# Kernel tuning notes

Measured on AMD Instinct MI355X. Metric: run time of the kernel, lower is better.

Reference implementation:

```python
import jax, jax.numpy as jnp
import numpy as np

B, N, DIM = 4, 4096, 1024
HEADS, DFF, WIN = 16, 4096, 128
EPS = 1e-5


def _layernorm(x, w, b):
    mu = jnp.mean(x, axis=-1, keepdims=True)
    var = jnp.mean(jnp.square(x - mu), axis=-1, keepdims=True)
    return (x - mu) * jax.lax.rsqrt(var + EPS) * w + b


def _local_attention(q, k, v, window):
    # q,k,v: (B, h, N, d); non-causal, look_backward=1, look_forward=1
    Bq, h, n, d = q.shape
    nb = n // window
    scale = d ** -0.5
    q = q.reshape(Bq * h, nb, window, d) * scale
    k = k.reshape(Bq * h, nb, window, d)
    v = v.reshape(Bq * h, nb, window, d)

    def look_around(t):  # (BH, nb, w, d) -> (BH, nb, 3w, d)
        tp = jnp.pad(t, ((0, 0), (1, 1), (0, 0), (0, 0)))
        return jnp.concatenate([tp[:, :-2], tp[:, 1:-1], tp[:, 2:]], axis=2)

    kk = look_around(k)
    vv = look_around(v)

    # validity mask for out-of-range look-around buckets
    idx = jnp.arange(n).reshape(nb, window)
    idx_p = jnp.pad(idx, ((1, 1), (0, 0)), constant_values=-1)
    kidx = jnp.concatenate([idx_p[:-2], idx_p[1:-1], idx_p[2:]], axis=1)  # (nb, 3w)
    valid = (kidx >= 0)[None, :, None, :]  # (1, nb, 1, 3w)

    sim = jnp.einsum('bnid,bnjd->bnij', q, kk)  # (BH, nb, w, 3w)
    neg = jnp.finfo(sim.dtype).min
    sim = jnp.where(valid, sim, neg)
    attn = jax.nn.softmax(sim, axis=-1)
    out = jnp.einsum('bnij,bnjd->bnid', attn, vv)
    return out.reshape(Bq, h, n, d)


def setup_inputs() -> dict:
    key = jax.random.key(0)
    ks = jax.random.split(key, 8)
    w = lambda k, shape: jax.random.normal(k, shape, jnp.float32) * 0.02
    return {
        'x': jax.random.normal(ks[0], (B, N, DIM), jnp.float32),
        'ln1_w': jnp.ones((DIM,), jnp.float32), 'ln1_b': jnp.zeros((DIM,), jnp.float32),
        'qkv_w': w(ks[1], (3 * DIM, DIM)), 'qkv_b': jnp.zeros((3 * DIM,), jnp.float32),
        'proj_w': w(ks[2], (DIM, DIM)), 'proj_b': jnp.zeros((DIM,), jnp.float32),
        'ln2_w': jnp.ones((DIM,), jnp.float32), 'ln2_b': jnp.zeros((DIM,), jnp.float32),
        'fc1_w': w(ks[3], (DFF, DIM)), 'fc1_b': jnp.zeros((DFF,), jnp.float32),
        'fc2_w': w(ks[4], (DIM, DFF)), 'fc2_b': jnp.zeros((DIM,), jnp.float32),
    }


def reference(x, ln1_w, ln1_b, qkv_w, qkv_b, proj_w, proj_b, ln2_w, ln2_b, fc1_w, fc1_b, fc2_w, fc2_b):
    Bx, n, C = x.shape
    h = HEADS
    hd = C // h
    x_norm = _layernorm(x, ln1_w, ln1_b)
    qkv = x_norm @ qkv_w.T + qkv_b  # (B, N, 3C)
    qkv = qkv.reshape(Bx, n, 3, h, hd).transpose(2, 0, 3, 1, 4)  # (3, B, h, N, hd)
    q, k, v = qkv[0], qkv[1], qkv[2]
    attn_out = _local_attention(q, k, v, WIN)  # (B, h, N, hd)
    attn_out = attn_out.transpose(0, 2, 1, 3).reshape(Bx, n, C)
    x = x + (attn_out @ proj_w.T + proj_b)
    y = _layernorm(x, ln2_w, ln2_b)
    y = jax.nn.gelu(y @ fc1_w.T + fc1_b, approximate=False)
    x = x + (y @ fc2_w.T + fc2_b)
    return x
```

## Files before the change

### kernel.cpp

```cpp
#include <hip/hip_runtime.h>
#include <math.h>

typedef unsigned short u16;
typedef __attribute__((ext_vector_type(4))) float f32x4;
typedef __attribute__((ext_vector_type(8))) __bf16 bf16x8;
typedef __attribute__((ext_vector_type(8))) u16 u16x8;
typedef __attribute__((ext_vector_type(4))) u16 u16x4;

__device__ __forceinline__ float bf2f(u16 v) {
    unsigned int u = ((unsigned int)v) << 16;
    return __builtin_bit_cast(float, u);
}
__device__ __forceinline__ u16 f2bf(float f) {
    unsigned int x = __builtin_bit_cast(unsigned int, f);
    x += 0x7fffu + ((x >> 16) & 1u);
    return (u16)(x >> 16);
}

__device__ __forceinline__ void load_lds16(const u16* g, u16* l) {
    __builtin_amdgcn_global_load_lds((const __attribute__((address_space(1))) void*)g,
                                     (__attribute__((address_space(3))) void*)l, 16, 0, 0);
}

#define WAIT_VM(N) asm volatile("s_waitcnt vmcnt(" #N ")" ::: "memory")
#define MFMA16(d, x, y) d = __builtin_amdgcn_mfma_f32_16x16x32_bf16(x, y, d, 0, 0, 0)

__device__ __forceinline__ void phase_barrier() {
    __builtin_amdgcn_sched_barrier(0);
    asm volatile("" ::: "memory");
    __builtin_amdgcn_s_barrier();
    asm volatile("" ::: "memory");
    __builtin_amdgcn_sched_barrier(0);
}

__global__ __launch_bounds__(256) void cvt_kernel(const float* __restrict__ in,
                                                  u16* __restrict__ out, int n)
{
    const int i = (blockIdx.x * 256 + threadIdx.x) * 4;
    if (i >= n) return;
    const float4 f = *(const float4*)(in + i);
    u16x4 o;
    o[0] = f2bf(f.x); o[1] = f2bf(f.y); o[2] = f2bf(f.z); o[3] = f2bf(f.w);
    *(u16x4*)(out + i) = o;
}

template<int EPI, int RES, bool OF32>
__global__ __launch_bounds__(512, 2) void gemm256(
    const u16* __restrict__ A, const u16* __restrict__ W,
    const float* __restrict__ bias,
    const float* __restrict__ resf, const u16* __restrict__ resb,
    void* __restrict__ O0v, u16* __restrict__ O1, u16* __restrict__ O2,
    int M, int N, int K, int mbase)
{
    __shared__ u16 S[65536];
    const int tid  = threadIdx.x;
    const int w    = tid >> 6;
    const int l    = tid & 63;
    const int colq = l & 15;
    const int quad = l >> 4;
    const int w3   = w & 3;
    const int wm   = (w >> 2) * 128;
    const int wn   = w3 * 64;

    const int nX  = (int)gridDim.x;
    const int nwg = nX * (int)gridDim.y;
    const int did = (int)blockIdx.y * nX + (int)blockIdx.x;
    const int q8  = nwg >> 3;
    const int wg  = (nwg & 7) ? did : ((did & 7) * q8 + (did >> 3));
    const int bm  = wg / nX;
    const int bn  = wg - bm * nX;
    const int m0  = bm * 256, n0 = bn * 256;

    const int rw   = l >> 3;
    const int sseg = ((l & 7) ^ rw) * 8;
    const u16* gA[2][2];
    const u16* gB[2][2];
#pragma unroll
    for (int h = 0; h < 2; ++h)
#pragma unroll
        for (int j = 0; j < 2; ++j) {
            const int rr = (w * 2 + j) * 8 + rw;
            gA[h][j] = A + (size_t)(m0 + h * 128 + rr) * K + sseg;
            const int nl = (rr >> 5) * 64 + (h * 2 + ((rr >> 4) & 1)) * 16 + (rr & 15);
            gB[h][j] = W + (size_t)(n0 + nl) * K + sseg;
        }
    const int lw = w * 1024;

    const int c0   = (quad * 8) ^ ((colq & 7) << 3);
    const int c1   = c0 ^ 32;
    const int aoff = (wm + colq) * 64;
    const int boff = 16384 + (w3 * 32 + colq) * 64;

    f32x4 acc[8][4] = {};
    bf16x8 a0[8], a1[8], b0, b1;

#pragma unroll
    for (int h = 0; h < 2; ++h)
#pragma unroll
        for (int j = 0; j < 2; ++j)
            load_lds16(gA[h][j], S + h * 8192 + lw + j * 512);
#pragma unroll
    for (int h = 0; h < 2; ++h)
#pragma unroll
        for (int j = 0; j < 2; ++j)
            load_lds16(gB[h][j], S + 16384 + h * 8192 + lw + j * 512);
    WAIT_VM(2);
    phase_barrier();

    const int NT = K >> 6;
    for (int t = 0; t < NT; ++t) {
        u16* Sc = S + ((t & 1) << 15);
        u16* Sn = S + (((t + 1) & 1) << 15);
        const int  kk = (t + 1) << 6;
        const bool pf = (t + 1) < NT;

#pragma unroll
        for (int mf = 0; mf < 8; ++mf)
            a0[mf] = *(const bf16x8*)(Sc + aoff + mf * 1024 + c0);
        b0 = *(const bf16x8*)(Sc + boff + c0);
        b1 = *(const bf16x8*)(Sc + boff + 1024 + c0);
        if (pf) {
#pragma unroll
            for (int h = 0; h < 2; ++h)
#pragma unroll
                for (int j = 0; j < 2; ++j)
                    load_lds16(gA[h][j] + kk, Sn + h * 8192 + lw + j * 512);
        }
        __builtin_amdgcn_s_setprio(1);
#pragma unroll
        for (int mf = 0; mf < 8; ++mf) { MFMA16(acc[mf][0], a0[mf], b0); MFMA16(acc[mf][1], a0[mf], b1); }
        __builtin_amdgcn_s_setprio(0);
        phase_barrier();

#pragma unroll
        for (int mf = 0; mf < 8; ++mf)
            a1[mf] = *(const bf16x8*)(Sc + aoff + mf * 1024 + c1);
        b0 = *(const bf16x8*)(Sc + boff + c1);
        b1 = *(const bf16x8*)(Sc + boff + 1024 + c1);
        if (pf) {
#pragma unroll
            for (int j = 0; j < 2; ++j)
                load_lds16(gB[0][j] + kk, Sn + 16384 + lw + j * 512);
        }
        __builtin_amdgcn_s_setprio(1);
#pragma unroll
        for (int mf = 0; mf < 8; ++mf) { MFMA16(acc[mf][0], a1[mf], b0); MFMA16(acc[mf][1], a1[mf], b1); }
        __builtin_amdgcn_s_setprio(0);
        if (pf) { WAIT_VM(6); } else { WAIT_VM(0); }
        phase_barrier();

        b0 = *(const bf16x8*)(Sc + boff + 8192 + c0);
        b1 = *(const bf16x8*)(Sc + boff + 8192 + 1024 + c0);
        if (pf) {
#pragma unroll
            for (int j = 0; j < 2; ++j)
                load_lds16(gB[1][j] + kk, Sn + 16384 + 8192 + lw + j * 512);
        }
        __builtin_amdgcn_s_setprio(1);
#pragma unroll
        for (int mf = 0; mf < 8; ++mf) { MFMA16(acc[mf][2], a0[mf], b0); MFMA16(acc[mf][3], a0[mf], b1); }
        __builtin_amdgcn_s_setprio(0);
        phase_barrier();

        b0 = *(const bf16x8*)(Sc + boff + 8192 + c1);
        b1 = *(const bf16x8*)(Sc + boff + 8192 + 1024 + c1);
        __builtin_amdgcn_s_setprio(1);
#pragma unroll
        for (int mf = 0; mf < 8; ++mf) { MFMA16(acc[mf][2], a1[mf], b0); MFMA16(acc[mf][3], a1[mf], b1); }
        __builtin_amdgcn_s_setprio(0);
        if (pf) { WAIT_VM(2); }
        phase_barrier();
    }

#pragma unroll
    for (int nf = 0; nf < 4; ++nf) {
        const int c = n0 + wn + nf * 16 + colq;
        const float bz = bias[c];
#pragma unroll
        for (int mf = 0; mf < 8; ++mf) {
#pragma unroll
            for (int i = 0; i < 4; ++i) {
                const int r = m0 + wm + mf * 16 + quad * 4 + i;
                float v = acc[mf][nf][i] + bz;
                if constexpr (EPI == 0) {
                    const int which = c >> 10;
                    const int head  = (c >> 6) & 15;
                    const int d     = c & 63;
                    const int rg    = mbase + r;
                    const int bb    = rg >> 12;
                    const int tt    = rg & 4095;
                    const int bh    = bb * 16 + head;
                    const u16 val = f2bf(v);
                    if (which == 0)      ((u16*)O0v)[((size_t)bh * 4096 + tt) * 64 + d] = val;
                    else if (which == 1) O1[((size_t)bh * 4096 + tt) * 64 + d] = val;
                    else                 O2[((size_t)bh * 64 + d) * 4096 + tt] = val;
                } else {
                    const size_t idx = (size_t)r * N + c;
                    if constexpr (RES == 1) v += resf[idx];
                    if constexpr (RES == 2) v += bf2f(resb[idx]);
                    if constexpr (EPI == 2) v = 0.5f * v * (1.0f + erff(v * 0.70710678118654752f));
                    if constexpr (OF32) ((float*)O0v)[idx] = v;
                    else                ((u16*)O0v)[idx] = f2bf(v);
                }
            }
        }
    }
}

template<bool F32IN>
__global__ __launch_bounds__(256) void ln_kernel(
    const void* __restrict__ xin, const float* __restrict__ w,
    const float* __restrict__ b, u16* __restrict__ out)
{
    const int wave = threadIdx.x >> 6, lane = threadIdx.x & 63;
    const size_t row = (size_t)blockIdx.x * 4 + wave;
    float v[16];
    if constexpr (F32IN) {
        const float* xr = (const float*)xin + row * 1024 + lane * 16;
#pragma unroll
        for (int j = 0; j < 4; ++j) {
            const float4 f = *(const float4*)(xr + j * 4);
            v[j * 4 + 0] = f.x; v[j * 4 + 1] = f.y; v[j * 4 + 2] = f.z; v[j * 4 + 3] = f.w;
        }
    } else {
        const u16* xr = (const u16*)xin + row * 1024 + lane * 16;
        u16x8 xa = *(const u16x8*)xr;
        u16x8 xb = *(const u16x8*)(xr + 8);
#pragma unroll
        for (int i = 0; i < 8; ++i) { v[i] = bf2f(xa[i]); v[8 + i] = bf2f(xb[i]); }
    }
    float s = 0.f, s2 = 0.f;
#pragma unroll
    for (int i = 0; i < 16; ++i) { s += v[i]; s2 += v[i] * v[i]; }
#pragma unroll
    for (int m = 32; m >= 1; m >>= 1) { s += __shfl_xor(s, m, 64); s2 += __shfl_xor(s2, m, 64); }
    const float mu  = s * (1.0f / 1024.0f);
    const float var = s2 * (1.0f / 1024.0f) - mu * mu;
    const float rs  = rsqrtf(var + 1e-5f);
    const float* wp = w + lane * 16;
    const float* bp = b + lane * 16;
    u16x8 oa, ob;
#pragma unroll
    for (int i = 0; i < 8; ++i) {
        oa[i] = f2bf((v[i]     - mu) * rs * wp[i]     + bp[i]);
        ob[i] = f2bf((v[8 + i] - mu) * rs * wp[8 + i] + bp[8 + i]);
    }
    u16* orow = out + row * 1024 + lane * 16;
    *(u16x8*)orow       = oa;
    *(u16x8*)(orow + 8) = ob;
}

__global__ __launch_bounds__(256, 4) void attn_kernel(
    const u16* __restrict__ Q, const u16* __restrict__ Kb,
    const u16* __restrict__ Vt, u16* __restrict__ out)
{
    __shared__ u16 Ps[4][16 * 200];
    const int tid  = threadIdx.x;
    const int wave = tid >> 6;
    const int lane = tid & 63;
    const int colq = lane & 15;
    const int quad = lane >> 4;

    const int f   = blockIdx.x;
    const int xcd = f & 7;
    const int s8  = f >> 3;
    const int bh  = s8 >> 3;
    const int tb  = (s8 & 7) + 8 * xcd;
    const int qrow0 = tb * 64 + wave * 16;
    const int nb    = tb >> 1;
    const int key0  = nb * 128 - 128;
    const int nt_lo = (nb == 0) ? 8 : 0;
    const int nt_hi = (nb == 31) ? 16 : 24;

    const u16* qp = Q + ((size_t)bh * 4096 + qrow0 + colq) * 64 + quad * 8;
    bf16x8 aq0 = *(const bf16x8*)qp;
    bf16x8 aq1 = *(const bf16x8*)(qp + 32);

    float m_i[4], l_i[4];
    f32x4 o[4] = {};
#pragma unroll
    for (int i = 0; i < 4; ++i) { m_i[i] = -3.0e38f; l_i[i] = 0.f; }

    u16* Psw = &Ps[wave][0];

#pragma unroll
    for (int c = 0; c < 2; ++c) {
        const int lo = (c == 0) ? nt_lo : 12;
        const int hi = (c == 0) ? ((nt_hi < 12) ? nt_hi : 12) : nt_hi;

        f32x4 sc[12];
#pragma unroll
        for (int j = 0; j < 12; ++j) sc[j] = (f32x4){0.f, 0.f, 0.f, 0.f};
#pragma unroll
        for (int j = 0; j < 12; ++j) {
            const int nt = c * 12 + j;
            if (nt >= lo && nt < hi) {
                const u16* kp = Kb + ((size_t)bh * 4096 + key0 + nt * 16 + colq) * 64 + quad * 8;
                bf16x8 b0 = *(const bf16x8*)kp;
                bf16x8 b1 = *(const bf16x8*)(kp + 32);
                f32x4 z = {0.f, 0.f, 0.f, 0.f};
                z = __builtin_amdgcn_mfma_f32_16x16x32_bf16(aq0, b0, z, 0, 0, 0);
                z = __builtin_amdgcn_mfma_f32_16x16x32_bf16(aq1, b1, z, 0, 0, 0);
                sc[j] = z;
            }
        }
        float mc[4];
#pragma unroll
        for (int i = 0; i < 4; ++i) mc[i] = -3.0e38f;
#pragma unroll
        for (int j = 0; j < 12; ++j) {
            const int nt = c * 12 + j;
            if (nt >= lo && nt < hi)
#pragma unroll
                for (int i = 0; i < 4; ++i) mc[i] = fmaxf(mc[i], sc[j][i]);
        }
#pragma unroll
        for (int i = 0; i < 4; ++i)
#pragma unroll
            for (int m = 8; m >= 1; m >>= 1) mc[i] = fmaxf(mc[i], __shfl_xor(mc[i], m, 64));
        float a_i[4], psum[4];
#pragma unroll
        for (int i = 0; i < 4; ++i) {
            const float mn = fmaxf(m_i[i], mc[i]);
            a_i[i] = __expf((m_i[i] - mn) * 0.125f);
            m_i[i] = mn;
            psum[i] = 0.f;
        }
#pragma unroll
        for (int j = 0; j < 12; ++j) {
            const int nt = c * 12 + j;
            if (nt >= lo && nt < hi) {
#pragma unroll
                for (int i = 0; i < 4; ++i) {
                    const float p = __expf((sc[j][i] - m_i[i]) * 0.125f);
                    psum[i] += p;
                    Psw[(quad * 4 + i) * 200 + j * 16 + colq] = f2bf(p);
                }
            }
        }
#pragma unroll
        for (int i = 0; i < 4; ++i)
#pragma unroll
            for (int m = 8; m >= 1; m >>= 1) psum[i] += __shfl_xor(psum[i], m, 64);
#pragma unroll
        for (int i = 0; i < 4; ++i) l_i[i] = l_i[i] * a_i[i] + psum[i];
#pragma unroll
        for (int dt = 0; dt < 4; ++dt)
#pragma unroll
            for (int i = 0; i < 4; ++i) o[dt][i] *= a_i[i];
        const int klo = (lo - c * 12) >> 1;
        const int khi = (hi - c * 12) >> 1;
#pragma unroll
        for (int k6 = 0; k6 < 6; ++k6) {
            if (k6 >= klo && k6 < khi) {
                bf16x8 ap = *(const bf16x8*)(Psw + colq * 200 + k6 * 32 + quad * 8);
                const int kkk = key0 + (c * 6 + k6) * 32 + quad * 8;
#pragma unroll
                for (int dt = 0; dt < 4; ++dt) {
                    const u16* vp = Vt + ((size_t)bh * 64 + dt * 16 + colq) * 4096 + kkk;
                    bf16x8 bv = *(const bf16x8*)vp;
                    o[dt] = __builtin_amdgcn_mfma_f32_16x16x32_bf16(ap, bv, o[dt], 0, 0, 0);
                }
            }
        }
    }

    const int bb = bh >> 4, hh = bh & 15;
#pragma unroll
    for (int i = 0; i < 4; ++i) {
        const float inv = 1.0f / fmaxf(l_i[i], 1e-20f);
        const int t = qrow0 + quad * 4 + i;
        u16* op = out + ((size_t)(bb * 4096 + t)) * 1024 + hh * 64;
#pragma unroll
        for (int dt = 0; dt < 4; ++dt) op[dt * 16 + colq] = f2bf(o[dt][i] * inv);
    }
}

extern "C" void kernel_launch(void* const* d_in, const int* in_sizes, int n_in,
                              void* d_out, int out_size, void* d_ws, size_t ws_size,
                              hipStream_t stream)
{
    const float* x      = (const float*)d_in[0];
    const float* ln1_w  = (const float*)d_in[1];
    const float* ln1_b  = (const float*)d_in[2];
    const float* qkv_w  = (const float*)d_in[3];
    const float* qkv_b  = (const float*)d_in[4];
    const float* proj_w = (const float*)d_in[5];
    const float* proj_b = (const float*)d_in[6];
    const float* ln2_w  = (const float*)d_in[7];
    const float* ln2_b  = (const float*)d_in[8];
    const float* fc1_w  = (const float*)d_in[9];
    const float* fc1_b  = (const float*)d_in[10];
    const float* fc2_w  = (const float*)d_in[11];
    const float* fc2_b  = (const float*)d_in[12];
    float* outp = (float*)d_out;

    if (ws_size < 134217728u) return;
    char* ws = (char*)d_ws;
    u16* R0 = (u16*)(ws);
    u16* R1 = (u16*)(ws + 33554432);
    u16* R2 = (u16*)(ws + 67108864);
    u16* R3 = (u16*)(ws + 100663296);
    u16* xnc    = (u16*)d_out;
    u16* attn_o = (u16*)((char*)d_out + 33554432);

    u16* qkvwb = R0;
    u16* projwb = R0 + 3145728;
    u16* fc1wb = R0 + 4194304;
    u16* fc2wb = R0 + 8388608;
    u16* Qb = R1, *Kb = R2, *Vtb = R3;
    u16* x2 = R1;
    u16* yn = attn_o;
    u16* hb = R2;

    cvt_kernel<<<3072, 256, 0, stream>>>(qkv_w, qkvwb, 3145728);
    cvt_kernel<<<1024, 256, 0, stream>>>(proj_w, projwb, 1048576);
    cvt_kernel<<<4096, 256, 0, stream>>>(fc1_w, fc1wb, 4194304);
    cvt_kernel<<<4096, 256, 0, stream>>>(fc2_w, fc2wb, 4194304);
    ln_kernel<true><<<4096, 256, 0, stream>>>(x, ln1_w, ln1_b, xnc);
    gemm256<0, 0, false><<<dim3(12, 64), 512, 0, stream>>>(xnc, qkvwb, qkv_b, nullptr, nullptr,
                                                           Qb, Kb, Vtb, 16384, 3072, 1024, 0);
    attn_kernel<<<4096, 256, 0, stream>>>(Qb, Kb, Vtb, attn_o);
    gemm256<1, 1, false><<<dim3(4, 64), 512, 0, stream>>>(attn_o, projwb, proj_b, x, nullptr,
                                                          x2, nullptr, nullptr, 16384, 1024, 1024, 0);
    ln_kernel<false><<<4096, 256, 0, stream>>>(x2, ln2_w, ln2_b, yn);
    for (int ci = 0; ci < 2; ++ci) {
        const size_t off = (size_t)ci * 8192 * 1024;
        gemm256<2, 0, false><<<dim3(16, 32), 512, 0, stream>>>(yn + off, fc1wb, fc1_b, nullptr, nullptr,
                                                               hb, nullptr, nullptr, 8192, 4096, 1024, 0);
        gemm256<1, 2, true><<<dim3(4, 32), 512, 0, stream>>>(hb, fc2wb, fc2_b, nullptr, x2 + off,
                                                             outp + off, nullptr, nullptr, 8192, 1024, 4096, 0);
    }
}
```

Before: 1.033 ms.

## Restructure GEMM K-loop phases, stage V-transpose via LDS, split MLP along hidden dimension

The GEMM inner loop now loads each A/B fragment quadrant once per k-tile, covering both k-halves, and issues four MFMA phases over quadrant pairs. Explicit lgkmcnt waits with plain s_barrier replace the old phase barriers. The QKV epilogue for V tiles goes through LDS so the transposed V output is written with contiguous 16-byte stores instead of scattered 2-byte stores. The MLP is split into four 1024-wide hidden chunks over all rows, with fc2 accumulating into the fp32 output through a residual read-modify-write. This needs lda/ldw parameters and different workspace aliasing, and it adds extra output traffic for the partial-sum accumulation.

```diff
diff --git a/kernel.cpp b/kernel.cpp
--- a/kernel.cpp
+++ b/kernel.cpp
@@ -23,15 +23,9 @@
 }
 
 #define WAIT_VM(N) asm volatile("s_waitcnt vmcnt(" #N ")" ::: "memory")
+#define LGKM0_SB() do { asm volatile("s_waitcnt lgkmcnt(0)" ::: "memory"); \
+                        __builtin_amdgcn_sched_barrier(0); } while (0)
 #define MFMA16(d, x, y) d = __builtin_amdgcn_mfma_f32_16x16x32_bf16(x, y, d, 0, 0, 0)
-
-__device__ __forceinline__ void phase_barrier() {
-    __builtin_amdgcn_sched_barrier(0);
-    asm volatile("" ::: "memory");
-    __builtin_amdgcn_s_barrier();
-    asm volatile("" ::: "memory");
-    __builtin_amdgcn_sched_barrier(0);
-}
 
 __global__ __launch_bounds__(256) void cvt_kernel(const float* __restrict__ in,
                                                   u16* __restrict__ out, int n)
@@ -50,7 +44,7 @@
     const float* __restrict__ bias,
     const float* __restrict__ resf, const u16* __restrict__ resb,
     void* __restrict__ O0v, u16* __restrict__ O1, u16* __restrict__ O2,
-    int M, int N, int K, int mbase)
+    int M, int N, int K, int lda, int ldw, int mbase)
 {
     __shared__ u16 S[65536];
     const int tid  = threadIdx.x;
@@ -79,33 +73,29 @@
     for (int h = 0; h < 2; ++h)
 #pragma unroll
         for (int j = 0; j < 2; ++j) {
-            const int rr = (w * 2 + j) * 8 + rw;
-            gA[h][j] = A + (size_t)(m0 + h * 128 + rr) * K + sseg;
+            const int rr = w * 16 + j * 8 + rw;
+            gA[h][j] = A + (size_t)(m0 + h * 128 + rr) * lda + sseg;
             const int nl = (rr >> 5) * 64 + (h * 2 + ((rr >> 4) & 1)) * 16 + (rr & 15);
-            gB[h][j] = W + (size_t)(n0 + nl) * K + sseg;
+            gB[h][j] = W + (size_t)(n0 + nl) * ldw + sseg;
         }
     const int lw = w * 1024;
 
-    const int c0   = (quad * 8) ^ ((colq & 7) << 3);
-    const int c1   = c0 ^ 32;
-    const int aoff = (wm + colq) * 64;
-    const int boff = 16384 + (w3 * 32 + colq) * 64;
+    const int c0 = (quad * 8) ^ ((colq & 7) << 3);
+    const int c1 = c0 ^ 32;
 
     f32x4 acc[8][4] = {};
-    bf16x8 a0[8], a1[8], b0, b1;
 
 #pragma unroll
     for (int h = 0; h < 2; ++h)
 #pragma unroll
         for (int j = 0; j < 2; ++j)
             load_lds16(gA[h][j], S + h * 8192 + lw + j * 512);
-#pragma unroll
-    for (int h = 0; h < 2; ++h)
-#pragma unroll
-        for (int j = 0; j < 2; ++j)
-            load_lds16(gB[h][j], S + 16384 + h * 8192 + lw + j * 512);
+    load_lds16(gB[0][0], S + 16384 + lw);
+    load_lds16(gB[0][1], S + 16384 + lw + 512);
+    load_lds16(gB[1][0], S + 16384 + 8192 + lw);
+    load_lds16(gB[1][1], S + 16384 + 8192 + lw + 512);
     WAIT_VM(2);
-    phase_barrier();
+    __builtin_amdgcn_s_barrier();
 
     const int NT = K >> 6;
     for (int t = 0; t < NT; ++t) {
@@ -114,11 +104,20 @@
         const int  kk = (t + 1) << 6;
         const bool pf = (t + 1) < NT;
 
-#pragma unroll
-        for (int mf = 0; mf < 8; ++mf)
-            a0[mf] = *(const bf16x8*)(Sc + aoff + mf * 1024 + c0);
-        b0 = *(const bf16x8*)(Sc + boff + c0);
-        b1 = *(const bf16x8*)(Sc + boff + 1024 + c0);
+        bf16x8 aL[4][2], aH[4][2], bL[2][2], bH[2][2];
+
+#pragma unroll
+        for (int m = 0; m < 4; ++m) {
+            const int rb = (wm + m * 16 + colq) * 64;
+            aL[m][0] = *(const bf16x8*)(Sc + rb + c0);
+            aL[m][1] = *(const bf16x8*)(Sc + rb + c1);
+        }
+#pragma unroll
+        for (int n = 0; n < 2; ++n) {
+            const int rb = 16384 + (w3 * 32 + n * 16 + colq) * 64;
+            bL[n][0] = *(const bf16x8*)(Sc + rb + c0);
+            bL[n][1] = *(const bf16x8*)(Sc + rb + c1);
+        }
         if (pf) {
 #pragma unroll
             for (int h = 0; h < 2; ++h)
@@ -126,56 +125,118 @@
                 for (int j = 0; j < 2; ++j)
                     load_lds16(gA[h][j] + kk, Sn + h * 8192 + lw + j * 512);
         }
+        __builtin_amdgcn_s_barrier();
+        LGKM0_SB();
         __builtin_amdgcn_s_setprio(1);
 #pragma unroll
-        for (int mf = 0; mf < 8; ++mf) { MFMA16(acc[mf][0], a0[mf], b0); MFMA16(acc[mf][1], a0[mf], b1); }
+        for (int m = 0; m < 4; ++m)
+#pragma unroll
+            for (int n = 0; n < 2; ++n) {
+                MFMA16(acc[m][n], aL[m][0], bL[n][0]);
+                MFMA16(acc[m][n], aL[m][1], bL[n][1]);
+            }
         __builtin_amdgcn_s_setprio(0);
-        phase_barrier();
-
-#pragma unroll
-        for (int mf = 0; mf < 8; ++mf)
-            a1[mf] = *(const bf16x8*)(Sc + aoff + mf * 1024 + c1);
-        b0 = *(const bf16x8*)(Sc + boff + c1);
-        b1 = *(const bf16x8*)(Sc + boff + 1024 + c1);
+        if (pf) { WAIT_VM(4); } else { WAIT_VM(0); }
+        __builtin_amdgcn_s_barrier();
+
+#pragma unroll
+        for (int n = 0; n < 2; ++n) {
+            const int rb = 16384 + 8192 + (w3 * 32 + n * 16 + colq) * 64;
+            bH[n][0] = *(const bf16x8*)(Sc + rb + c0);
+            bH[n][1] = *(const bf16x8*)(Sc + rb + c1);
+        }
         if (pf) {
-#pragma unroll
-            for (int j = 0; j < 2; ++j)
-                load_lds16(gB[0][j] + kk, Sn + 16384 + lw + j * 512);
-        }
+            load_lds16(gB[0][0] + kk, Sn + 16384 + lw);
+            load_lds16(gB[0][1] + kk, Sn + 16384 + lw + 512);
+        }
+        __builtin_amdgcn_s_barrier();
+        LGKM0_SB();
         __builtin_amdgcn_s_setprio(1);
 #pragma unroll
-        for (int mf = 0; mf < 8; ++mf) { MFMA16(acc[mf][0], a1[mf], b0); MFMA16(acc[mf][1], a1[mf], b1); }
+        for (int m = 0; m < 4; ++m)
+#pragma unroll
+            for (int n = 0; n < 2; ++n) {
+                MFMA16(acc[m][2 + n], aL[m][0], bH[n][0]);
+                MFMA16(acc[m][2 + n], aL[m][1], bH[n][1]);
+            }
         __builtin_amdgcn_s_setprio(0);
-        if (pf) { WAIT_VM(6); } else { WAIT_VM(0); }
-        phase_barrier();
-
-        b0 = *(const bf16x8*)(Sc + boff + 8192 + c0);
-        b1 = *(const bf16x8*)(Sc + boff + 8192 + 1024 + c0);
+        __builtin_amdgcn_s_barrier();
+
+#pragma unroll
+        for (int m = 0; m < 4; ++m) {
+            const int rb = (wm + 64 + m * 16 + colq) * 64;
+            aH[m][0] = *(const bf16x8*)(Sc + rb + c0);
+            aH[m][1] = *(const bf16x8*)(Sc + rb + c1);
+        }
         if (pf) {
-#pragma unroll
-            for (int j = 0; j < 2; ++j)
-                load_lds16(gB[1][j] + kk, Sn + 16384 + 8192 + lw + j * 512);
-        }
+            load_lds16(gB[1][0] + kk, Sn + 16384 + 8192 + lw);
+            load_lds16(gB[1][1] + kk, Sn + 16384 + 8192 + lw + 512);
+        }
+        __builtin_amdgcn_s_barrier();
+        LGKM0_SB();
         __builtin_amdgcn_s_setprio(1);
 #pragma unroll
-        for (int mf = 0; mf < 8; ++mf) { MFMA16(acc[mf][2], a0[mf], b0); MFMA16(acc[mf][3], a0[mf], b1); }
+        for (int m = 0; m < 4; ++m)
+#pragma unroll
+            for (int n = 0; n < 2; ++n) {
+                MFMA16(acc[4 + m][n], aH[m][0], bL[n][0]);
+                MFMA16(acc[4 + m][n], aH[m][1], bL[n][1]);
+            }
         __builtin_amdgcn_s_setprio(0);
-        phase_barrier();
-
-        b0 = *(const bf16x8*)(Sc + boff + 8192 + c1);
-        b1 = *(const bf16x8*)(Sc + boff + 8192 + 1024 + c1);
+        __builtin_amdgcn_s_barrier();
+
         __builtin_amdgcn_s_setprio(1);
 #pragma unroll
-        for (int mf = 0; mf < 8; ++mf) { MFMA16(acc[mf][2], a1[mf], b0); MFMA16(acc[mf][3], a1[mf], b1); }
+        for (int m = 0; m < 4; ++m)
+#pragma unroll
+            for (int n = 0; n < 2; ++n) {
+                MFMA16(acc[4 + m][2 + n], aH[m][0], bH[n][0]);
+                MFMA16(acc[4 + m][2 + n], aH[m][1], bH[n][1]);
+            }
         __builtin_amdgcn_s_setprio(0);
         if (pf) { WAIT_VM(2); }
-        phase_barrier();
-    }
-
+        __builtin_amdgcn_s_barrier();
+    }
+
+    if constexpr (EPI == 0) {
+        if (n0 >= 2048) {
+            __syncthreads();
+#pragma unroll
+            for (int nf = 0; nf < 4; ++nf) {
+                const int cl = wn + nf * 16 + colq;
+                const float bz = bias[n0 + cl];
+                const int swz = (cl & 7) << 3;
+#pragma unroll
+                for (int mf = 0; mf < 8; ++mf) {
+                    const int rb = wm + mf * 16 + quad * 4;
+                    u16x4 pk;
+#pragma unroll
+                    for (int i = 0; i < 4; ++i) pk[i] = f2bf(acc[mf][nf][i] + bz);
+                    *(u16x4*)(S + cl * 256 + (rb ^ swz)) = pk;
+                }
+            }
+            __syncthreads();
+            const int cl   = tid >> 1;
+            const int c    = n0 + cl;
+            const int head = (c >> 6) & 15;
+            const int d    = c & 63;
+            const int rg0  = mbase + m0;
+            const int bh   = (rg0 >> 12) * 16 + head;
+            const int half = tid & 1;
+            const int swz  = (cl & 7) << 3;
+            u16* op = O2 + ((size_t)bh * 64 + d) * 4096 + (rg0 & 4095) + half * 128;
+#pragma unroll
+            for (int j = 0; j < 16; ++j) {
+                const int r0 = half * 128 + j * 8;
+                *(u16x8*)(op + j * 8) = *(const u16x8*)(S + cl * 256 + (r0 ^ swz));
+            }
+            return;
+        }
+    }
 #pragma unroll
     for (int nf = 0; nf < 4; ++nf) {
         const int c = n0 + wn + nf * 16 + colq;
-        const float bz = bias[c];
+        const float bz = bias ? bias[c] : 0.f;
 #pragma unroll
         for (int mf = 0; mf < 8; ++mf) {
 #pragma unroll
@@ -183,17 +244,14 @@
                 const int r = m0 + wm + mf * 16 + quad * 4 + i;
                 float v = acc[mf][nf][i] + bz;
                 if constexpr (EPI == 0) {
-                    const int which = c >> 10;
-                    const int head  = (c >> 6) & 15;
-                    const int d     = c & 63;
-                    const int rg    = mbase + r;
-                    const int bb    = rg >> 12;
-                    const int tt    = rg & 4095;
-                    const int bh    = bb * 16 + head;
+                    const int head = (c >> 6) & 15;
+                    const int d    = c & 63;
+                    const int rg   = mbase + r;
+                    const int tt   = rg & 4095;
+                    const int bh   = (rg >> 12) * 16 + head;
                     const u16 val = f2bf(v);
-                    if (which == 0)      ((u16*)O0v)[((size_t)bh * 4096 + tt) * 64 + d] = val;
-                    else if (which == 1) O1[((size_t)bh * 4096 + tt) * 64 + d] = val;
-                    else                 O2[((size_t)bh * 64 + d) * 4096 + tt] = val;
+                    if (c < 1024) ((u16*)O0v)[((size_t)bh * 4096 + tt) * 64 + d] = val;
+                    else          O1[((size_t)bh * 4096 + tt) * 64 + d] = val;
                 } else {
                     const size_t idx = (size_t)r * N + c;
                     if constexpr (RES == 1) v += resf[idx];
@@ -401,34 +459,42 @@
     u16* R1 = (u16*)(ws + 33554432);
     u16* R2 = (u16*)(ws + 67108864);
     u16* R3 = (u16*)(ws + 100663296);
-    u16* xnc    = (u16*)d_out;
-    u16* attn_o = (u16*)((char*)d_out + 33554432);
-
-    u16* qkvwb = R0;
+    u16* attn_o = (u16*)d_out;
+    u16* xnc    = (u16*)((char*)d_out + 33554432);
+
+    u16* qkvwb  = R0;
     u16* projwb = R0 + 3145728;
-    u16* fc1wb = R0 + 4194304;
-    u16* fc2wb = R0 + 8388608;
+    u16* fc1wb  = R0 + 4194304;
+    u16* fc2wb  = R0 + 8388608;
     u16* Qb = R1, *Kb = R2, *Vtb = R3;
     u16* x2 = R1;
-    u16* yn = attn_o;
-    u16* hb = R2;
+    u16* yn = R2;
+    u16* hc = R3;
 
     cvt_kernel<<<3072, 256, 0, stream>>>(qkv_w, qkvwb, 3145728);
     cvt_kernel<<<1024, 256, 0, stream>>>(proj_w, projwb, 1048576);
     cvt_kernel<<<4096, 256, 0, stream>>>(fc1_w, fc1wb, 4194304);
     cvt_kernel<<<4096, 256, 0, stream>>>(fc2_w, fc2wb, 4194304);
     ln_kernel<true><<<4096, 256, 0, stream>>>(x, ln1_w, ln1_b, xnc);
-    gemm256<0, 0, false><<<dim3(12, 64), 512, 0, stream>>>(xnc, qkvwb, qkv_b, nullptr, nullptr,
-                                                           Qb, Kb, Vtb, 16384, 3072, 1024, 0);
+    gemm256<0, 0, false><<<dim3(12, 64), 512, 0, stream>>>(
+        xnc, qkvwb, qkv_b, nullptr, nullptr, Qb, Kb, Vtb,
+        16384, 3072, 1024, 1024, 1024, 0);
     attn_kernel<<<4096, 256, 0, stream>>>(Qb, Kb, Vtb, attn_o);
-    gemm256<1, 1, false><<<dim3(4, 64), 512, 0, stream>>>(attn_o, projwb, proj_b, x, nullptr,
-                                                          x2, nullptr, nullptr, 16384, 1024, 1024, 0);
+    gemm256<1, 1, false><<<dim3(4, 64), 512, 0, stream>>>(
+        attn_o, projwb, proj_b, x, nullptr, x2, nullptr, nullptr,
+        16384, 1024, 1024, 1024, 1024, 0);
     ln_kernel<false><<<4096, 256, 0, stream>>>(x2, ln2_w, ln2_b, yn);
-    for (int ci = 0; ci < 2; ++ci) {
-        const size_t off = (size_t)ci * 8192 * 1024;
-        gemm256<2, 0, false><<<dim3(16, 32), 512, 0, stream>>>(yn + off, fc1wb, fc1_b, nullptr, nullptr,
-                                                               hb, nullptr, nullptr, 8192, 4096, 1024, 0);
-        gemm256<1, 2, true><<<dim3(4, 32), 512, 0, stream>>>(hb, fc2wb, fc2_b, nullptr, x2 + off,
-                                                             outp + off, nullptr, nullptr, 8192, 1024, 4096, 0);
-    }
-}
+    for (int c = 0; c < 4; ++c) {
+        gemm256<2, 0, false><<<dim3(4, 64), 512, 0, stream>>>(
+            yn, fc1wb + (size_t)c * 1048576, fc1_b + c * 1024, nullptr, nullptr,
+            hc, nullptr, nullptr, 16384, 1024, 1024, 1024, 1024, 0);
+        if (c == 0)
+            gemm256<1, 2, true><<<dim3(4, 64), 512, 0, stream>>>(
+                hc, fc2wb, fc2_b, nullptr, x2, outp, nullptr, nullptr,
+                16384, 1024, 1024, 1024, 4096, 0);
+        else
+            gemm256<1, 1, true><<<dim3(4, 64), 512, 0, stream>>>(
+                hc, fc2wb + c * 1024, nullptr, outp, nullptr, outp, nullptr, nullptr,
+                16384, 1024, 1024, 1024, 4096, 0);
+    }
+}
```

Measured after the change: 1.033 ms. Within noise of the previous version (+0.1%).
